# Optimization experiments

Hardware: AMD Instinct MI355X
Metric: run time of the kernel (lower is better)

Reference implementation:

```python
import jax, jax.numpy as jnp
import numpy as np

NC = 5        # num_class
NS = 2        # n_sigma
MAX_ID = 3    # candidate instance ids per class: 1..MAX_ID
W_INST, W_VAR, W_SEED = 1.0, 10.0, 1.0
GRID = 1024   # size of the registered xym buffer
H = W = 768
CLASS_WEIGHT = np.ones((NC,), np.float32)


def _xym(h, w):
    # buffer built at GRID resolution, then sliced [0:h, 0:w] (matches torch)
    base = jnp.linspace(0.0, 1.0, GRID)
    xm = jnp.broadcast_to(base[None, :w], (h, w))  # x varies along width
    ym = jnp.broadcast_to(base[:h, None], (h, w))  # y varies along height
    return jnp.stack([xm, ym], 0)  # [2,h,w]


def _lovasz_flat(logits, labels_f):
    # standard flat Lovasz hinge
    signs = 2.0 * labels_f - 1.0
    errors = 1.0 - logits * signs
    perm = jnp.argsort(-errors)  # descending errors
    errors_sorted = errors[perm]
    gt_sorted = labels_f[perm]
    gts = jnp.sum(gt_sorted)
    inter = gts - jnp.cumsum(gt_sorted)
    union = gts + jnp.cumsum(1.0 - gt_sorted)
    jac = 1.0 - inter / union
    jac = jnp.concatenate([jac[:1], jac[1:] - jac[:-1]])
    return jnp.dot(jax.nn.relu(errors_sorted), jax.lax.stop_gradient(jac))


def _per_image(pred, inst, lab, xyf, cw):
    h, w = lab.shape
    n = h * w
    embf = jnp.tanh(pred[0:2]).reshape(2, n) + xyf          # spatial embedding [2,N]
    sigf = pred[2:2 + NS].reshape(NS, n)                     # sigma [NS,N]
    seedf = jax.nn.sigmoid(pred[2 + NS:2 + NS + NC]).reshape(NC, n)  # seed maps [NC,N]
    labf = lab.reshape(n)
    instf = inst.reshape(n)

    cls = jnp.arange(1, NC + 1)
    # background seed loss per class: sum(seed^2) over pixels where label != cl
    bg = labf[None, :] != cls[:, None]
    seed_bg = jnp.sum(jnp.where(bg, seedf, 0.0) ** 2)

    cl_pair = jnp.repeat(cls, MAX_ID)                       # [P]
    id_pair = jnp.tile(jnp.arange(1, MAX_ID + 1), NC)       # [P]

    def per_inst(cl, iid):
        ci = cl - 1
        m = (labf == cl) & (instf == iid)                   # [N]
        mf = m.astype(embf.dtype)
        cnt = jnp.sum(mf)
        valid = cnt > 0
        cnts = jnp.maximum(cnt, 1.0)
        # approximate medoid: per-dim lower median of masked coords,
        # then masked pixel closest to the median
        xy_sorted = jnp.sort(jnp.where(m[None, :], xyf, 2.0), axis=1)
        mid = jnp.maximum((cnt.astype(jnp.int32) - 1) // 2, 0)
        med = jnp.take(xy_sorted, mid, axis=1)              # [2]
        d = jnp.sum((xyf - med[:, None]) ** 2, axis=0)
        imin = jnp.argmin(jnp.where(m, d, jnp.inf))
        center = jnp.take(xyf, imin, axis=1)                # [2], constant wrt params
        s_mean = jnp.sum(sigf * mf[None, :], axis=1) / cnts  # [NS]
        var = jnp.sum(mf[None, :] * (sigf - jax.lax.stop_gradient(s_mean)[:, None]) ** 2) / (cnts * NS)
        s = jnp.exp(s_mean * 10.0)                           # [NS]
        dist = jnp.exp(-jnp.sum((embf - center[:, None]) ** 2 * s[:, None], axis=0))  # [N]
        lov = _lovasz_flat(dist * 2.0 - 1.0, mf)
        seedc = jnp.take(seedf, ci, axis=0)
        seed_in = jnp.sum(mf * (seedc - jax.lax.stop_gradient(dist)) ** 2)
        return valid, var, lov, seed_in

    valid, var, lov, seed_in = jax.vmap(per_inst)(cl_pair, id_pair)
    vf = valid.astype(embf.dtype)
    objs = jnp.maximum(jnp.sum(vf), 1.0)
    w_pair = jnp.take(cw, cl_pair - 1)
    seed_loss = (seed_bg + jnp.sum(w_pair * seed_in * vf)) / n
    return (W_INST * jnp.sum(lov * vf) / objs
            + W_VAR * jnp.sum(var * vf) / objs
            + W_SEED * seed_loss)


def setup_inputs() -> dict:
    key = jax.random.key(0)
    k1, k2, k3 = jax.random.split(key, 3)
    prediction = jax.random.normal(k1, (2, 2 + NS + NC, H, W), dtype=jnp.float32)
    instances = jax.random.randint(k2, (2, H, W), 0, MAX_ID + 1, dtype=jnp.int32)
    labels = jax.random.randint(k3, (2, H, W), 0, NC + 1, dtype=jnp.int32)
    return {"prediction": prediction, "instances": instances, "labels": labels}


def reference(prediction, instances, labels):
    xyf = _xym(H, W).reshape(2, H * W)
    cw = jnp.asarray(CLASS_WEIGHT)
    losses = jax.vmap(lambda p, i, l: _per_image(p, i, l, xyf, cw))(prediction, instances, labels)
    return jnp.mean(losses)
```

## Files before the change

### kernel.cpp

```cpp
#include <hip/hip_runtime.h>
#include <cstddef>
#include <cstdint>


#define HH 768
#define WW 768
#define NPIX (HH*WW)
#define NCL 5
#define MAXID 3
#define PAIRS (NCL*MAXID)
#define NIMG 2
#define NCH 9
#define BINS 256
#define NSH 8
#define HPXB 1152
#define HNB (NPIX/HPXB)
#define TX 12
#define TY 32
#define XW 64
#define YH 24
#define BPI (TX*TY)
#define ANB 64
#define APXB (NPIX/ANB)

struct WS {
  alignas(8) unsigned int hall8[NSH][NIMG][PAIRS][2][BINS];
  float seedpart[NIMG][PAIRS][64];
  unsigned int lovdone;
  unsigned int zpad0;
  unsigned long long argkey[NIMG][PAIRS];
  float varsum[NIMG][PAIRS];
  float seedin[NIMG][PAIRS];
  float medx[NIMG][PAIRS], medy[NIMG][PAIRS];
  float s0a[NIMG][PAIRS], s1a[NIMG][PAIRS];
  float sm0a[NIMG][PAIRS], sm1a[NIMG][PAIRS];
  float validf[NIMG][PAIRS], cntf[NIMG][PAIRS];
  float lov[NIMG][PAIRS];
  float seedT[NIMG], seedOwn[NIMG];
  unsigned int cnt[NIMG][PAIRS];
  alignas(16) float4 emb4[NIMG][NPIX];
  unsigned char pridx[NIMG][NPIX];
  alignas(64) unsigned short colpart[NIMG][PAIRS][WW][TY];
  alignas(64) unsigned short rowpart[NIMG][PAIRS][HH][TX];
  float sig0part[NIMG][PAIRS][BPI];
  float sig1part[NIMG][PAIRS][BPI];
  float sq0part[NIMG][PAIRS][BPI];
  float sq1part[NIMG][PAIRS][BPI];
  float sTpart[NIMG][BPI];
  float sOpart[NIMG][BPI];
};

__device__ __forceinline__ float basef(int i) {
  return (float)i * (1.0f / 1023.0f);
}
__device__ __forceinline__ int pair_of(int l, int it) {
  return (l >= 1 && l <= NCL && it >= 1 && it <= MAXID) ? (l - 1) * MAXID + (it - 1) : -1;
}
__device__ __forceinline__ float fast_sigmoid(float z) {
  return __fdividef(1.f, 1.f + __expf(-z));
}
__device__ __forceinline__ float fast_tanh(float x) {
  float xc = fminf(fmaxf(x, -15.f), 15.f);
  float e = __expf(2.f * xc);
  return __fdividef(e - 1.f, e + 1.f);
}

__global__ __launch_bounds__(256) void k_pass1(const float* __restrict__ pred,
                                               const int* __restrict__ inst,
                                               const int* __restrict__ lab,
                                               WS* __restrict__ ws) {
  int img = blockIdx.z;
  int xt = blockIdx.x, yt = blockIdx.y;
  int x0 = xt * XW;
  int y0 = yt * YH;
  int tid = threadIdx.x, lane = tid & 63, wv = tid >> 6;

  {
    const int ZN = (int)(offsetof(WS, argkey) / 4);
    int bid = (blockIdx.z * TY + blockIdx.y) * TX + blockIdx.x;
    int idx = bid * 256 + tid;
    if (idx < ZN) ((unsigned int*)ws)[idx] = 0u;
    if (bid == 0 && tid < NIMG * PAIRS)
      ((unsigned long long*)ws->argkey)[tid] = ~0ULL;
  }

  const float* p = pred + (size_t)img * NCH * NPIX;
  const int* lb = lab + (size_t)img * NPIX;
  const int* ib = inst + (size_t)img * NPIX;

  __shared__ unsigned int lcol[PAIRS][XW];
  __shared__ unsigned int lrow[PAIRS][YH];
  __shared__ float lsig0[PAIRS], lsig1[PAIRS], lsq0[PAIRS], lsq1[PAIRS];
  __shared__ float fred0[4], fred1[4];
  for (int k = tid; k < PAIRS * XW; k += 256) ((unsigned int*)lcol)[k] = 0;
  for (int k = tid; k < PAIRS * YH; k += 256) ((unsigned int*)lrow)[k] = 0;
  if (tid < PAIRS) { lsig0[tid] = 0.f; lsig1[tid] = 0.f; lsq0[tid] = 0.f; lsq1[tid] = 0.f; }
  __syncthreads();

  int x = x0 + lane;
  float bx = basef(x);
  float t = 0.f, own = 0.f;
#pragma unroll
  for (int i = 0; i < YH / 4; i++) {
    int y = y0 + wv + 4 * i;
    int pix = y * WW + x;
    int l = lb[pix];
    int it = ib[pix];
    float s, q, sdown = 0.f;
    s = fast_sigmoid(p[4 * NPIX + pix]); q = s * s; t += q; if (l == 1) { own += q; sdown = s; }
    s = fast_sigmoid(p[5 * NPIX + pix]); q = s * s; t += q; if (l == 2) { own += q; sdown = s; }
    s = fast_sigmoid(p[6 * NPIX + pix]); q = s * s; t += q; if (l == 3) { own += q; sdown = s; }
    s = fast_sigmoid(p[7 * NPIX + pix]); q = s * s; t += q; if (l == 4) { own += q; sdown = s; }
    s = fast_sigmoid(p[8 * NPIX + pix]); q = s * s; t += q; if (l == 5) { own += q; sdown = s; }
    float e0 = fast_tanh(p[0 * NPIX + pix]) + bx;
    float e1 = fast_tanh(p[1 * NPIX + pix]) + basef(y);
    int pr = pair_of(l, it);
    float4 rec;
    rec.x = e0; rec.y = e1; rec.z = sdown;
    rec.w = __int_as_float(pr >= 0 ? pr : 255);
    ws->emb4[img][pix] = rec;
    ws->pridx[img][pix] = (unsigned char)(pr >= 0 ? pr : 255);
    if (pr >= 0) {
      float g0 = p[2 * NPIX + pix];
      float g1 = p[3 * NPIX + pix];
      atomicAdd(&lcol[pr][lane], 1u);
      atomicAdd(&lrow[pr][y - y0], 1u);
      atomicAdd(&lsig0[pr], g0);
      atomicAdd(&lsig1[pr], g1);
      atomicAdd(&lsq0[pr], g0 * g0);
      atomicAdd(&lsq1[pr], g1 * g1);
    }
  }
  for (int o = 32; o; o >>= 1) { t += __shfl_down(t, o); own += __shfl_down(own, o); }
  if (lane == 0) { fred0[wv] = t; fred1[wv] = own; }
  __syncthreads();

  int bi = yt * TX + xt;
  for (int k = tid; k < PAIRS * XW; k += 256) {
    int pp = k >> 6, c = k & 63;
    ws->colpart[img][pp][x0 + c][yt] = (unsigned short)lcol[pp][c];
  }
  for (int k = tid; k < PAIRS * YH; k += 256) {
    int pp = k / YH, r = k % YH;
    ws->rowpart[img][pp][y0 + r][xt] = (unsigned short)lrow[pp][r];
  }
  if (tid < PAIRS) {
    ws->sig0part[img][tid][bi] = lsig0[tid];
    ws->sig1part[img][tid][bi] = lsig1[tid];
    ws->sq0part[img][tid][bi] = lsq0[tid];
    ws->sq1part[img][tid][bi] = lsq1[tid];
  }
  if (tid == 0) {
    ws->sTpart[img][bi] = fred0[0] + fred0[1] + fred0[2] + fred0[3];
    ws->sOpart[img][bi] = fred1[0] + fred1[1] + fred1[2] + fred1[3];
  }
}

__global__ __launch_bounds__(256) void k_medoid(WS* __restrict__ ws) {
  int img = blockIdx.x / PAIRS, p = blockIdx.x % PAIRS;
  int tid = threadIdx.x, lane = tid & 63, wv = tid >> 6;
  __shared__ unsigned int pref[256];
  __shared__ int cross;
  __shared__ float fr0[4], fr1[4], fr2[4], fr3[4];
  unsigned int c = 0;
  int res[2];
#pragma unroll
  for (int h = 0; h < 2; h++) {
    unsigned int v[3];
#pragma unroll
    for (int j = 0; j < 3; j++) {
      int cc = tid * 3 + j;
      unsigned int s = 0;
      if (h == 0) {
        const unsigned int* w = (const unsigned int*)ws->colpart[img][p][cc];
#pragma unroll
        for (int i = 0; i < TY / 2; i++) { unsigned int u = w[i]; s += (u & 0xFFFFu) + (u >> 16); }
      } else {
        const unsigned int* w = (const unsigned int*)ws->rowpart[img][p][cc];
#pragma unroll
        for (int i = 0; i < TX / 2; i++) { unsigned int u = w[i]; s += (u & 0xFFFFu) + (u >> 16); }
      }
      v[j] = s;
    }
    unsigned int s3 = v[0] + v[1] + v[2];
    pref[tid] = s3;
    __syncthreads();
    for (int d = 1; d < 256; d <<= 1) {
      unsigned int tv = (tid >= d) ? pref[tid - d] : 0u;
      __syncthreads();
      pref[tid] += tv;
      __syncthreads();
    }
    c = pref[255];
    unsigned int target = (c > 0) ? (((c - 1u) >> 1) + 1u) : 1u;
    if (tid == 0) cross = 0;
    __syncthreads();
    unsigned int inc = pref[tid];
    unsigned int exc = inc - s3;
    if (inc >= target && exc < target) {
      int j = (exc + v[0] >= target) ? 0 : ((exc + v[0] + v[1] >= target) ? 1 : 2);
      cross = tid * 3 + j;
    }
    __syncthreads();
    res[h] = cross;
    __syncthreads();
  }
  float s0 = 0.f, s1 = 0.f, q0 = 0.f, q1 = 0.f;
  for (int b = tid; b < BPI; b += 256) {
    s0 += ws->sig0part[img][p][b]; s1 += ws->sig1part[img][p][b];
    q0 += ws->sq0part[img][p][b];  q1 += ws->sq1part[img][p][b];
  }
  for (int o = 32; o; o >>= 1) {
    s0 += __shfl_down(s0, o); s1 += __shfl_down(s1, o);
    q0 += __shfl_down(q0, o); q1 += __shfl_down(q1, o);
  }
  if (lane == 0) { fr0[wv] = s0; fr1[wv] = s1; fr2[wv] = q0; fr3[wv] = q1; }
  __syncthreads();
  if (tid == 0) {
    float sig0 = fr0[0] + fr0[1] + fr0[2] + fr0[3];
    float sig1 = fr1[0] + fr1[1] + fr1[2] + fr1[3];
    float sq0 = fr2[0] + fr2[1] + fr2[2] + fr2[3];
    float sq1 = fr3[0] + fr3[1] + fr3[2] + fr3[3];
    float vf = (c > 0) ? 1.f : 0.f;
    float cf = (c > 0) ? (float)c : 1.f;
    float sm0 = sig0 / cf, sm1 = sig1 / cf;
    ws->cnt[img][p] = c;
    ws->medx[img][p] = basef(res[0]);
    ws->medy[img][p] = basef(res[1]);
    ws->sm0a[img][p] = sm0;
    ws->sm1a[img][p] = sm1;
    ws->s0a[img][p] = __expf(10.f * sm0);
    ws->s1a[img][p] = __expf(10.f * sm1);
    ws->validf[img][p] = vf;
    ws->cntf[img][p] = cf;
    ws->varsum[img][p] = (sq0 - cf * sm0 * sm0) + (sq1 - cf * sm1 * sm1);
  }
  __syncthreads();
  if (p == 0) {
    float a = 0.f, o2 = 0.f;
    for (int b = tid; b < BPI; b += 256) { a += ws->sTpart[img][b]; o2 += ws->sOpart[img][b]; }
    for (int o = 32; o; o >>= 1) { a += __shfl_down(a, o); o2 += __shfl_down(o2, o); }
    if (lane == 0) { fr0[wv] = a; fr1[wv] = o2; }
    __syncthreads();
    if (tid == 0) {
      ws->seedT[img] = fr0[0] + fr0[1] + fr0[2] + fr0[3];
      ws->seedOwn[img] = fr1[0] + fr1[1] + fr1[2] + fr1[3];
    }
  }
}

__global__ __launch_bounds__(256) void k_argmin(WS* __restrict__ ws) {
  int img = blockIdx.y;
  __shared__ unsigned long long skey[PAIRS];
  __shared__ float smx[PAIRS], smy[PAIRS];
  if (threadIdx.x < PAIRS) {
    skey[threadIdx.x] = ~0ULL;
    smx[threadIdx.x] = ws->medx[img][threadIdx.x];
    smy[threadIdx.x] = ws->medy[img][threadIdx.x];
  }
  __syncthreads();
  int base = blockIdx.x * APXB;
#pragma unroll
  for (int i = 0; i < APXB / 1024; i++) {
    int px0 = base + i * 1024 + threadIdx.x * 4;
    uchar4 pr4 = *(const uchar4*)(ws->pridx[img] + px0);
    int y = px0 / WW;
    int x0 = px0 - y * WW;
    float by = basef(y);
#pragma unroll
    for (int k = 0; k < 4; k++) {
      int pr = (k == 0) ? pr4.x : (k == 1) ? pr4.y : (k == 2) ? pr4.z : pr4.w;
      if (pr != 255) {
        int pix = px0 + k;
        float dx = basef(x0 + k) - smx[pr];
        float dy = by - smy[pr];
        float d = dx * dx + dy * dy;
        unsigned long long key = ((unsigned long long)__float_as_uint(d) << 32) | (unsigned int)pix;
        atomicMin(&skey[pr], key);
      }
    }
  }
  __syncthreads();
  if (threadIdx.x < PAIRS && skey[threadIdx.x] != ~0ULL)
    atomicMin(&ws->argkey[img][threadIdx.x], skey[threadIdx.x]);
}

__global__ __launch_bounds__(512) void k_hist(WS* __restrict__ ws) {
  int img = blockIdx.y;
  int tid = threadIdx.x;
  __shared__ unsigned int h32[PAIRS * 2 * BINS];
  __shared__ float lseed[PAIRS];
  for (int k = tid; k < PAIRS * 2 * BINS; k += 512) h32[k] = 0;
  if (tid < PAIRS) lseed[tid] = 0.f;
  __syncthreads();

  float cxr[PAIRS], cyr[PAIRS], S0r[PAIRS], S1r[PAIRS];
#pragma unroll
  for (int p = 0; p < PAIRS; p++) {
    unsigned long long key = ws->argkey[img][p];
    int imin = (int)(key & 0xffffffffu);
    cxr[p] = basef(imin % WW);
    cyr[p] = basef(imin / WW);
    S0r[p] = ws->s0a[img][p];
    S1r[p] = ws->s1a[img][p];
  }
  const float4* eb = ws->emb4[img];
  int base = blockIdx.x * HPXB;

  auto hist_px = [&](float4 v) {
    int pp = __float_as_int(v.w);
    float dOwn = 0.f;
#pragma unroll
    for (int p = 0; p < PAIRS; p++) {
      float dx = v.x - cxr[p];
      float dy = v.y - cyr[p];
      float q = dx * dx * S0r[p] + dy * dy * S1r[p];
      float d = __expf(-q);
      bool m = (pp == p);
      dOwn = m ? d : dOwn;
      int ib2 = (int)fminf(d * 256.f, 255.f);
      atomicAdd(&h32[p * 512 + (ib2 ^ (m ? 511 : 0))], 1u);
    }
    if (pp != 255) { float sd = v.z - dOwn; atomicAdd(&lseed[pp], sd * sd); }
  };

  float4 vA = eb[base + tid];
  float4 vB = eb[base + 512 + tid];
  float4 vC;
  bool hasC = tid < (HPXB - 1024);
  if (hasC) vC = eb[base + 1024 + tid];
  hist_px(vA);
  hist_px(vB);
  if (hasC) hist_px(vC);
  __syncthreads();

  unsigned long long* gh = (unsigned long long*)&ws->hall8[blockIdx.x & (NSH - 1)][img][0][0][0];
  for (int k = tid; k < PAIRS * 2 * BINS / 2; k += 512) {
    unsigned int lo = h32[2 * k], hi = h32[2 * k + 1];
    if (lo | hi) {
      unsigned long long v = (unsigned long long)lo | ((unsigned long long)hi << 32);
      atomicAdd(&gh[k], v);
    }
  }
  if (tid < PAIRS && lseed[tid] != 0.f)
    atomicAdd(&ws->seedpart[img][tid][blockIdx.x & 63], lseed[tid]);
}

__global__ __launch_bounds__(256) void k_lovasz(WS* __restrict__ ws, float* __restrict__ out) {
  int b = blockIdx.x / PAIRS, p = blockIdx.x % PAIRS;
  unsigned int gts = ws->cnt[b][p];
  int tid = threadIdx.x;
  float lv = 0.f;
  __shared__ unsigned int sin_s[BINS], sout_s[BINS];
  if (gts != 0) {
    unsigned int si = 0, so = 0;
#pragma unroll
    for (int s = 0; s < NSH; s++) {
      si += ws->hall8[s][b][p][1][tid];
      so += ws->hall8[s][b][p][0][tid];
    }
    sin_s[tid] = si; sout_s[tid] = so;
    __syncthreads();
    for (int d = 1; d < BINS; d <<= 1) {
      unsigned int a = (tid + d < BINS) ? sin_s[tid + d] : 0u;
      unsigned int c = (tid + d < BINS) ? sout_s[tid + d] : 0u;
      __syncthreads();
      sin_s[tid] += a; sout_s[tid] += c;
      __syncthreads();
    }
    float gtsf = (float)gts;
    float js = 0.f;
    if (tid >= 1) {
      unsigned int Sin = sin_s[tid], Sout = sout_s[tid];
      js = 1.f - (float)(gts - Sin) / (gtsf + (float)Sout);
    }
    for (int o = 32; o; o >>= 1) js += __shfl_down(js, o);
    __shared__ float wsum[4];
    if ((tid & 63) == 0) wsum[tid >> 6] = js;
    __syncthreads();
    if (tid == 0)
      lv = (2.f / BINS) * (0.5f + wsum[0] + wsum[1] + wsum[2] + wsum[3]);
  }
  __shared__ float seedred;
  if (tid < 64) {
    float sv = ws->seedpart[b][p][tid];
    for (int o = 32; o; o >>= 1) sv += __shfl_down(sv, o);
    if (tid == 0) seedred = sv;
  }
  __syncthreads();
  __shared__ int amLast;
  if (tid == 0) {
    atomicExch(&ws->lov[b][p], lv);
    atomicExch(&ws->seedin[b][p], seedred);
    __threadfence();
    unsigned int old = atomicAdd(&ws->lovdone, 1u);
    amLast = (old == NIMG * PAIRS - 1);
  }
  __syncthreads();
  if (amLast) {
    __shared__ float rl[NIMG], rv[NIMG], rs[NIMG], ro[NIMG];
    if (tid < NIMG) { rl[tid] = 0.f; rv[tid] = 0.f; rs[tid] = 0.f; ro[tid] = 0.f; }
    __syncthreads();
    if (tid < NIMG * PAIRS) {
      int bb = tid / PAIRS, pp = tid % PAIRS;
      float vf = ws->validf[bb][pp];
      float lvv = atomicAdd(&ws->lov[bb][pp], 0.f);
      float sdv = atomicAdd(&ws->seedin[bb][pp], 0.f);
      atomicAdd(&rl[bb], vf * lvv);
      atomicAdd(&rv[bb], vf * ws->varsum[bb][pp] / (ws->cntf[bb][pp] * 2.f));
      atomicAdd(&rs[bb], vf * sdv);
      atomicAdd(&ro[bb], vf);
    }
    __syncthreads();
    if (tid == 0) {
      float tot = 0.f;
      for (int bb = 0; bb < NIMG; bb++) {
        float objs = ro[bb] < 1.f ? 1.f : ro[bb];
        float seed_bg = ws->seedT[bb] - ws->seedOwn[bb];
        float seed_loss = (seed_bg + rs[bb]) / (float)NPIX;
        tot += rl[bb] / objs + 10.f * rv[bb] / objs + seed_loss;
      }
      out[0] = tot * 0.5f;
    }
  }
}

extern "C" void kernel_launch(void* const* d_in, const int* in_sizes, int n_in,
                              void* d_out, int out_size, void* d_ws, size_t ws_size,
                              hipStream_t stream) {
  const float* pred = (const float*)d_in[0];
  const int* inst = (const int*)d_in[1];
  const int* lab = (const int*)d_in[2];
  WS* ws = (WS*)d_ws;

  k_pass1<<<dim3(TX, TY, NIMG), 256, 0, stream>>>(pred, inst, lab, ws);
  k_medoid<<<dim3(NIMG * PAIRS), 256, 0, stream>>>(ws);
  k_argmin<<<dim3(ANB, NIMG), 256, 0, stream>>>(ws);
  k_hist<<<dim3(HNB, NIMG), 512, 0, stream>>>(ws);
  k_lovasz<<<dim3(NIMG * PAIRS), 256, 0, stream>>>(ws, (float*)d_out);
}
```

Measured before the change: 79.88 us.

## Vectorize pass1 loads with float4 per thread and reshape tiles to 256x16

The first pass now has each thread handle four consecutive pixels, using float4/int4 loads for all nine prediction channels and both label maps and a packed uchar4 store for the pair index. The tile shape changes to 256 columns by 16 rows with 512 threads per block, so the medoid kernel's row-partial reduction now sums three shorts. The aim is fewer, wider global memory transactions in the bandwidth-bound first pass. The cost is higher register pressure, and shared-memory atomics on lcol now come from threads covering four columns each.

New measurement: 94.06 us. +17.8%, slower.

```diff
diff --git a/kernel.cpp b/kernel.cpp
--- a/kernel.cpp
+++ b/kernel.cpp
@@ -15,10 +15,10 @@
 #define NSH 8
 #define HPXB 1152
 #define HNB (NPIX/HPXB)
-#define TX 12
-#define TY 32
-#define XW 64
-#define YH 24
+#define XW 256
+#define YH 16
+#define TX 3
+#define TY 48
 #define BPI (TX*TY)
 #define ANB 64
 #define APXB (NPIX/ANB)
@@ -64,8 +64,14 @@
   float e = __expf(2.f * xc);
   return __fdividef(e - 1.f, e + 1.f);
 }
-
-__global__ __launch_bounds__(256) void k_pass1(const float* __restrict__ pred,
+__device__ __forceinline__ float vget(float4 v, int k) {
+  return (k == 0) ? v.x : (k == 1) ? v.y : (k == 2) ? v.z : v.w;
+}
+__device__ __forceinline__ int iget(int4 v, int k) {
+  return (k == 0) ? v.x : (k == 1) ? v.y : (k == 2) ? v.z : v.w;
+}
+
+__global__ __launch_bounds__(512) void k_pass1(const float* __restrict__ pred,
                                                const int* __restrict__ inst,
                                                const int* __restrict__ lab,
                                                WS* __restrict__ ws) {
@@ -78,7 +84,7 @@
   {
     const int ZN = (int)(offsetof(WS, argkey) / 4);
     int bid = (blockIdx.z * TY + blockIdx.y) * TX + blockIdx.x;
-    int idx = bid * 256 + tid;
+    int idx = bid * 512 + tid;
     if (idx < ZN) ((unsigned int*)ws)[idx] = 0u;
     if (bid == 0 && tid < NIMG * PAIRS)
       ((unsigned long long*)ws->argkey)[tid] = ~0ULL;
@@ -91,56 +97,71 @@
   __shared__ unsigned int lcol[PAIRS][XW];
   __shared__ unsigned int lrow[PAIRS][YH];
   __shared__ float lsig0[PAIRS], lsig1[PAIRS], lsq0[PAIRS], lsq1[PAIRS];
-  __shared__ float fred0[4], fred1[4];
-  for (int k = tid; k < PAIRS * XW; k += 256) ((unsigned int*)lcol)[k] = 0;
-  for (int k = tid; k < PAIRS * YH; k += 256) ((unsigned int*)lrow)[k] = 0;
+  __shared__ float fred0[8], fred1[8];
+  for (int k = tid; k < PAIRS * XW; k += 512) ((unsigned int*)lcol)[k] = 0;
+  for (int k = tid; k < PAIRS * YH; k += 512) ((unsigned int*)lrow)[k] = 0;
   if (tid < PAIRS) { lsig0[tid] = 0.f; lsig1[tid] = 0.f; lsq0[tid] = 0.f; lsq1[tid] = 0.f; }
   __syncthreads();
 
-  int x = x0 + lane;
-  float bx = basef(x);
+  int xq = lane;
   float t = 0.f, own = 0.f;
 #pragma unroll
-  for (int i = 0; i < YH / 4; i++) {
-    int y = y0 + wv + 4 * i;
-    int pix = y * WW + x;
-    int l = lb[pix];
-    int it = ib[pix];
-    float s, q, sdown = 0.f;
-    s = fast_sigmoid(p[4 * NPIX + pix]); q = s * s; t += q; if (l == 1) { own += q; sdown = s; }
-    s = fast_sigmoid(p[5 * NPIX + pix]); q = s * s; t += q; if (l == 2) { own += q; sdown = s; }
-    s = fast_sigmoid(p[6 * NPIX + pix]); q = s * s; t += q; if (l == 3) { own += q; sdown = s; }
-    s = fast_sigmoid(p[7 * NPIX + pix]); q = s * s; t += q; if (l == 4) { own += q; sdown = s; }
-    s = fast_sigmoid(p[8 * NPIX + pix]); q = s * s; t += q; if (l == 5) { own += q; sdown = s; }
-    float e0 = fast_tanh(p[0 * NPIX + pix]) + bx;
-    float e1 = fast_tanh(p[1 * NPIX + pix]) + basef(y);
-    int pr = pair_of(l, it);
-    float4 rec;
-    rec.x = e0; rec.y = e1; rec.z = sdown;
-    rec.w = __int_as_float(pr >= 0 ? pr : 255);
-    ws->emb4[img][pix] = rec;
-    ws->pridx[img][pix] = (unsigned char)(pr >= 0 ? pr : 255);
-    if (pr >= 0) {
-      float g0 = p[2 * NPIX + pix];
-      float g1 = p[3 * NPIX + pix];
-      atomicAdd(&lcol[pr][lane], 1u);
-      atomicAdd(&lrow[pr][y - y0], 1u);
-      atomicAdd(&lsig0[pr], g0);
-      atomicAdd(&lsig1[pr], g1);
-      atomicAdd(&lsq0[pr], g0 * g0);
-      atomicAdd(&lsq1[pr], g1 * g1);
-    }
+  for (int i = 0; i < 2; i++) {
+    int r = wv + 8 * i;
+    int y = y0 + r;
+    int pixb = y * WW + x0 + xq * 4;
+    float4 c0 = *(const float4*)(p + 0 * NPIX + pixb);
+    float4 c1 = *(const float4*)(p + 1 * NPIX + pixb);
+    float4 c2 = *(const float4*)(p + 2 * NPIX + pixb);
+    float4 c3 = *(const float4*)(p + 3 * NPIX + pixb);
+    float4 c4 = *(const float4*)(p + 4 * NPIX + pixb);
+    float4 c5 = *(const float4*)(p + 5 * NPIX + pixb);
+    float4 c6 = *(const float4*)(p + 6 * NPIX + pixb);
+    float4 c7 = *(const float4*)(p + 7 * NPIX + pixb);
+    float4 c8 = *(const float4*)(p + 8 * NPIX + pixb);
+    int4 l4 = *(const int4*)(lb + pixb);
+    int4 i4 = *(const int4*)(ib + pixb);
+    float by = basef(y);
+    uchar4 pv;
+#pragma unroll
+    for (int k = 0; k < 4; k++) {
+      int l = iget(l4, k), it = iget(i4, k);
+      float s, q, sdown = 0.f;
+      s = fast_sigmoid(vget(c4, k)); q = s * s; t += q; if (l == 1) { own += q; sdown = s; }
+      s = fast_sigmoid(vget(c5, k)); q = s * s; t += q; if (l == 2) { own += q; sdown = s; }
+      s = fast_sigmoid(vget(c6, k)); q = s * s; t += q; if (l == 3) { own += q; sdown = s; }
+      s = fast_sigmoid(vget(c7, k)); q = s * s; t += q; if (l == 4) { own += q; sdown = s; }
+      s = fast_sigmoid(vget(c8, k)); q = s * s; t += q; if (l == 5) { own += q; sdown = s; }
+      float e0 = fast_tanh(vget(c0, k)) + basef(x0 + xq * 4 + k);
+      float e1 = fast_tanh(vget(c1, k)) + by;
+      int pr = pair_of(l, it);
+      float4 rec;
+      rec.x = e0; rec.y = e1; rec.z = sdown;
+      rec.w = __int_as_float(pr >= 0 ? pr : 255);
+      ws->emb4[img][pixb + k] = rec;
+      ((unsigned char*)&pv)[k] = (unsigned char)(pr >= 0 ? pr : 255);
+      if (pr >= 0) {
+        float g0 = vget(c2, k), g1 = vget(c3, k);
+        atomicAdd(&lcol[pr][xq * 4 + k], 1u);
+        atomicAdd(&lrow[pr][r], 1u);
+        atomicAdd(&lsig0[pr], g0);
+        atomicAdd(&lsig1[pr], g1);
+        atomicAdd(&lsq0[pr], g0 * g0);
+        atomicAdd(&lsq1[pr], g1 * g1);
+      }
+    }
+    *(uchar4*)(ws->pridx[img] + pixb) = pv;
   }
   for (int o = 32; o; o >>= 1) { t += __shfl_down(t, o); own += __shfl_down(own, o); }
   if (lane == 0) { fred0[wv] = t; fred1[wv] = own; }
   __syncthreads();
 
   int bi = yt * TX + xt;
-  for (int k = tid; k < PAIRS * XW; k += 256) {
-    int pp = k >> 6, c = k & 63;
+  for (int k = tid; k < PAIRS * XW; k += 512) {
+    int pp = k >> 8, c = k & 255;
     ws->colpart[img][pp][x0 + c][yt] = (unsigned short)lcol[pp][c];
   }
-  for (int k = tid; k < PAIRS * YH; k += 256) {
+  for (int k = tid; k < PAIRS * YH; k += 512) {
     int pp = k / YH, r = k % YH;
     ws->rowpart[img][pp][y0 + r][xt] = (unsigned short)lrow[pp][r];
   }
@@ -151,8 +172,11 @@
     ws->sq1part[img][tid][bi] = lsq1[tid];
   }
   if (tid == 0) {
-    ws->sTpart[img][bi] = fred0[0] + fred0[1] + fred0[2] + fred0[3];
-    ws->sOpart[img][bi] = fred1[0] + fred1[1] + fred1[2] + fred1[3];
+    float a = 0.f, b2 = 0.f;
+#pragma unroll
+    for (int w = 0; w < 8; w++) { a += fred0[w]; b2 += fred1[w]; }
+    ws->sTpart[img][bi] = a;
+    ws->sOpart[img][bi] = b2;
   }
 }
 
@@ -176,9 +200,8 @@
 #pragma unroll
         for (int i = 0; i < TY / 2; i++) { unsigned int u = w[i]; s += (u & 0xFFFFu) + (u >> 16); }
       } else {
-        const unsigned int* w = (const unsigned int*)ws->rowpart[img][p][cc];
-#pragma unroll
-        for (int i = 0; i < TX / 2; i++) { unsigned int u = w[i]; s += (u & 0xFFFFu) + (u >> 16); }
+        const unsigned short* w = ws->rowpart[img][p][cc];
+        s = (unsigned int)w[0] + w[1] + w[2];
       }
       v[j] = s;
     }
@@ -433,7 +456,7 @@
   const int* lab = (const int*)d_in[2];
   WS* ws = (WS*)d_ws;
 
-  k_pass1<<<dim3(TX, TY, NIMG), 256, 0, stream>>>(pred, inst, lab, ws);
+  k_pass1<<<dim3(TX, TY, NIMG), 512, 0, stream>>>(pred, inst, lab, ws);
   k_medoid<<<dim3(NIMG * PAIRS), 256, 0, stream>>>(ws);
   k_argmin<<<dim3(ANB, NIMG), 256, 0, stream>>>(ws);
   k_hist<<<dim3(HNB, NIMG), 512, 0, stream>>>(ws);
```
